# Kernel optimization log

Measured on AMD Instinct MI355X. Metric: run time of the kernel, lower is better.

## Reference

```python
import jax, jax.numpy as jnp
import numpy as np

N = 50000
E = 1600000
F_IN = 512
NHID = 32
LATENT = 16
NCLS = 16


def setup_inputs() -> dict:
    key = jax.random.key(0)
    ks = jax.random.split(key, 10)
    return {
        "features": jax.random.normal(ks[0], (N, F_IN), dtype=jnp.float32),
        "edge_src": jax.random.randint(ks[1], (E,), 0, N, dtype=jnp.int32),
        "edge_dst": jax.random.randint(ks[2], (E,), 0, N, dtype=jnp.int32),
        "edge_weight": jax.random.uniform(ks[3], (E,), dtype=jnp.float32),
        "W1": jax.random.normal(ks[4], (F_IN, NHID), dtype=jnp.float32) / np.sqrt(F_IN),
        "W2": jax.random.normal(ks[5], (NHID, LATENT), dtype=jnp.float32) / np.sqrt(NHID),
        "W3": jax.random.normal(ks[6], (LATENT, NCLS), dtype=jnp.float32) / np.sqrt(LATENT),
        "W4": jax.random.normal(ks[7], (NCLS, LATENT), dtype=jnp.float32) / np.sqrt(NCLS),
        "W5": jax.random.normal(ks[8], (LATENT, NHID), dtype=jnp.float32) / np.sqrt(LATENT),
        "W6": jax.random.normal(ks[9], (NHID, F_IN), dtype=jnp.float32) / np.sqrt(NHID),
    }


def gcn_conv(x, W, src, dst, w):
    # support = x @ W ; out = A_hat @ support (sparse aggregation over edges)
    support = x @ W                       # [N, out]
    msg = support[src] * w[:, None]       # [E, out]
    return jax.ops.segment_sum(msg, dst, num_segments=N)


def reference(features, edge_src, edge_dst, edge_weight, W1, W2, W3, W4, W5, W6):
    # dropout p=0.0 (eval semantics) -> identity
    x1 = jnp.tanh(gcn_conv(features, W1, edge_src, edge_dst, edge_weight))
    x2 = jnp.tanh(gcn_conv(x1, W2, edge_src, edge_dst, edge_weight))
    z = jnp.tanh(gcn_conv(x2, W3, edge_src, edge_dst, edge_weight))
    z2 = jnp.tanh(gcn_conv(z, W4, edge_src, edge_dst, edge_weight)) + x2
    z1 = jnp.tanh(gcn_conv(z2, W5, edge_src, edge_dst, edge_weight)) + x1
    feat_recon = jax.nn.sigmoid(gcn_conv(z1, W6, edge_src, edge_dst, edge_weight))
    pred = jax.nn.softmax(z, axis=1)
    return feat_recon, z, pred
```

## Files before the change

kernel.cpp:

```cpp
#include <hip/hip_runtime.h>
#include <hip/hip_bf16.h>
#include <math.h>

#define FIN 512
#define NHID 32
#define LAT 16
#define BCAP 16384

#define BR 128
#define KC 64
__global__ __launch_bounds__(256) void gemm_fin(const float* __restrict__ feat,
                                                const float* __restrict__ W,
                                                float* __restrict__ out0,
                                                float* __restrict__ out1,
                                                int n, int ntile) {
    __shared__ float xT[KC][BR];
    __shared__ float Wc[KC][NHID];
    const int tid = threadIdx.x;
    const int tile = blockIdx.x % ntile;
    const int khalf = blockIdx.x / ntile;
    const int r0 = tile * BR;
    const int k0 = khalf * 256;
    float* __restrict__ out = khalf ? out1 : out0;
    const int rt = tid >> 3;
    const int ct = tid & 7;
    const int srow = tid >> 4;
    const int sc4 = tid & 15;
    float acc[4][4] = {{0.f}};

    for (int kc = 0; kc < 256; kc += KC) {
        {
            const float4* wg = reinterpret_cast<const float4*>(W + (k0 + kc) * NHID);
            float4* wl = reinterpret_cast<float4*>(&Wc[0][0]);
            wl[tid] = wg[tid];
            wl[tid + 256] = wg[tid + 256];
        }
#pragma unroll
        for (int i = 0; i < 8; ++i) {
            int rr = srow + 16 * i;
            int r = r0 + rr;
            float4 v;
            if (r < n)
                v = *reinterpret_cast<const float4*>(feat + (size_t)r * FIN + k0 + kc + sc4 * 4);
            else
                v.x = v.y = v.z = v.w = 0.f;
            int gs = ((rr >> 2) ^ (sc4 & 7)) * 4 + (rr & 3);
            xT[sc4 * 4 + 0][gs] = v.x;
            xT[sc4 * 4 + 1][gs] = v.y;
            xT[sc4 * 4 + 2][gs] = v.z;
            xT[sc4 * 4 + 3][gs] = v.w;
        }
        __syncthreads();
#pragma unroll 4
        for (int k = 0; k < KC; ++k) {
            int sw = (rt ^ ((k >> 2) & 7)) * 4;
            float4 xv = *reinterpret_cast<const float4*>(&xT[k][sw]);
            float4 wv = *reinterpret_cast<const float4*>(&Wc[k][ct * 4]);
            acc[0][0] = fmaf(xv.x, wv.x, acc[0][0]);
            acc[0][1] = fmaf(xv.x, wv.y, acc[0][1]);
            acc[0][2] = fmaf(xv.x, wv.z, acc[0][2]);
            acc[0][3] = fmaf(xv.x, wv.w, acc[0][3]);
            acc[1][0] = fmaf(xv.y, wv.x, acc[1][0]);
            acc[1][1] = fmaf(xv.y, wv.y, acc[1][1]);
            acc[1][2] = fmaf(xv.y, wv.z, acc[1][2]);
            acc[1][3] = fmaf(xv.y, wv.w, acc[1][3]);
            acc[2][0] = fmaf(xv.z, wv.x, acc[2][0]);
            acc[2][1] = fmaf(xv.z, wv.y, acc[2][1]);
            acc[2][2] = fmaf(xv.z, wv.z, acc[2][2]);
            acc[2][3] = fmaf(xv.z, wv.w, acc[2][3]);
            acc[3][0] = fmaf(xv.w, wv.x, acc[3][0]);
            acc[3][1] = fmaf(xv.w, wv.y, acc[3][1]);
            acc[3][2] = fmaf(xv.w, wv.z, acc[3][2]);
            acc[3][3] = fmaf(xv.w, wv.w, acc[3][3]);
        }
        __syncthreads();
    }
#pragma unroll
    for (int i = 0; i < 4; ++i) {
        int r = r0 + rt * 4 + i;
        if (r < n) {
            float4 o;
            o.x = acc[i][0]; o.y = acc[i][1]; o.z = acc[i][2]; o.w = acc[i][3];
            *reinterpret_cast<float4*>(out + (size_t)r * NHID + ct * 4) = o;
        }
    }
}

__global__ __launch_bounds__(256) void add2(float* __restrict__ a,
                                            const float* __restrict__ b, int n4) {
    int i = blockIdx.x * 256 + threadIdx.x;
    if (i < n4) {
        float4 va = reinterpret_cast<float4*>(a)[i];
        float4 vb = reinterpret_cast<const float4*>(b)[i];
        va.x += vb.x; va.y += vb.y; va.z += vb.z; va.w += vb.w;
        reinterpret_cast<float4*>(a)[i] = va;
    }
}

__global__ __launch_bounds__(256) void binit(int* __restrict__ bcursor, int nb) {
    int t = threadIdx.x;
    if (t < nb) bcursor[t] = t * BCAP;
}

__global__ __launch_bounds__(256) void build_a(const int* __restrict__ src,
                                               const int* __restrict__ dst,
                                               const float* __restrict__ w,
                                               int* __restrict__ bcursor,
                                               unsigned long long* __restrict__ rec2,
                                               int e, int nb) {
    __shared__ int cnt[256];
    __shared__ int gb[256];
    const int tid = threadIdx.x;
    const int i0 = blockIdx.x * 4096;
    cnt[tid] = 0;
    __syncthreads();
    unsigned long long rc[16];
    int rkbk[16];
#pragma unroll
    for (int k = 0; k < 16; ++k) {
        int j = i0 + k * 256 + tid;
        rkbk[k] = -1;
        if (j < e) {
            int d = dst[j];
            int b = d >> 8;
            int rk = atomicAdd(&cnt[b], 1);
            rkbk[k] = (rk << 8) | b;
            rc[k] = ((unsigned long long)__float_as_uint(w[j]) << 32) |
                    ((unsigned)d << 16) | (unsigned)src[j];
        }
    }
    __syncthreads();
    if (tid < nb && cnt[tid] > 0) gb[tid] = atomicAdd(&bcursor[tid], cnt[tid]);
    __syncthreads();
#pragma unroll
    for (int k = 0; k < 16; ++k) {
        if (rkbk[k] >= 0) {
            int b = rkbk[k] & 255;
            int rk = rkbk[k] >> 8;
            rec2[gb[b] + rk] = rc[k];
        }
    }
}

__global__ __launch_bounds__(256) void build_b(const unsigned long long* __restrict__ rec2,
                                               const int* __restrict__ bcursor,
                                               int2* __restrict__ rp2,
                                               unsigned long long* __restrict__ rec,
                                               int n) {
    __shared__ int cnt[256];
    __shared__ int cur[256];
    const int t = threadIdx.x;
    const int b = blockIdx.x;
    const int lo = b * BCAP;
    const int hi = bcursor[b];
    cnt[t] = 0;
    __syncthreads();
    for (int i = lo + t; i < hi; i += 256)
        atomicAdd(&cnt[((unsigned)rec2[i] >> 16) & 255], 1);
    __syncthreads();
    int v = cnt[t];
    cur[t] = v;
    __syncthreads();
    for (int off = 1; off < 256; off <<= 1) {
        int x = (t >= off) ? cur[t - off] : 0;
        __syncthreads();
        cur[t] += x;
        __syncthreads();
    }
    int ex = cur[t] - v;
    int node = b * 256 + t;
    if (node < n) {
        int2 se; se.x = lo + ex; se.y = lo + ex + v;
        rp2[node] = se;
    }
    __syncthreads();
    cur[t] = ex;
    __syncthreads();
    for (int i = lo + t; i < hi; i += 256) {
        unsigned long long r = rec2[i];
        unsigned lo32 = (unsigned)r;
        int ln = (lo32 >> 16) & 255;
        int p = atomicAdd(&cur[ln], 1);
        rec[lo + p] = (r & 0xffffffff00000000ull) | (lo32 & 0xffffu);
    }
}

template <int NE, bool PRED, int D>
__device__ __forceinline__ void gath(const float* __restrict__ sq,
                                     const unsigned long long* __restrict__ rec,
                                     int e0, int end,
                                     float& ax, float& ay, float& az, float& aw) {
    unsigned long long r[NE];
#pragma unroll
    for (int j = 0; j < NE; ++j)
        r[j] = (!PRED || (e0 + 4 * j < end)) ? rec[e0 + 4 * j] : 0ull;
    float4 v[NE];
#pragma unroll
    for (int j = 0; j < NE; ++j)
        v[j] = *reinterpret_cast<const float4*>(sq + (size_t)(unsigned)(r[j] & 0xffffffffu) * D);
#pragma unroll
    for (int j = 0; j < NE; ++j) {
        float w = __uint_as_float((unsigned)(r[j] >> 32));
        ax = fmaf(v[j].x, w, ax); ay = fmaf(v[j].y, w, ay);
        az = fmaf(v[j].z, w, az); aw = fmaf(v[j].w, w, aw);
    }
}

template <int D, int C, int MODE, bool SMAX>
__global__ __launch_bounds__(256) void agg_fused(const float* __restrict__ s,
                                                 const unsigned long long* __restrict__ rec,
                                                 const int2* __restrict__ rp2,
                                                 const float* __restrict__ Wn,
                                                 const float* __restrict__ res,
                                                 float* __restrict__ out0,
                                                 float* __restrict__ out1,
                                                 float* __restrict__ pred, int n) {
    constexpr int CH = D / 4;
    __shared__ float wl[(MODE == 1 || MODE == 3) ? D * C : 1];
    if (MODE == 1 || MODE == 3) {
        for (int i = threadIdx.x; i < D * C; i += 256) wl[i] = Wn[i];
        __syncthreads();
    }
    constexpr int NPB = 256 / D;
    const int node = blockIdx.x * NPB + threadIdx.x / D;
    const int lane = threadIdx.x % D;
    const int q = lane & (CH - 1);
    const int st = lane / CH;
    float ax = 0.f, ay = 0.f, az = 0.f, aw = 0.f;
    if (node < n) {
        const float* sq = s + 4 * q;
        int2 se = rp2[node];
        int i = se.x;
        const int end = se.y;
        for (; i + 32 <= end; i += 32)
            gath<8, false, D>(sq, rec, i + st, end, ax, ay, az, aw);
        if (i + 16 <= end) {
            gath<4, false, D>(sq, rec, i + st, end, ax, ay, az, aw);
            i += 16;
        }
        if (i < end)
            gath<4, true, D>(sq, rec, i + st, end, ax, ay, az, aw);
    }
    ax += __shfl_xor(ax, CH, D);  ax += __shfl_xor(ax, 2 * CH, D);
    ay += __shfl_xor(ay, CH, D);  ay += __shfl_xor(ay, 2 * CH, D);
    az += __shfl_xor(az, CH, D);  az += __shfl_xor(az, 2 * CH, D);
    aw += __shfl_xor(aw, CH, D);  aw += __shfl_xor(aw, 2 * CH, D);

    if (MODE == 1) {
        float vx = tanhf(ax), vy = tanhf(ay), vz = tanhf(az), vw = tanhf(aw);
        if (node < n && st == 0) {
            float4 o; o.x = vx; o.y = vy; o.z = vz; o.w = vw;
            *reinterpret_cast<float4*>(out0 + (size_t)node * D + 4 * q) = o;
        }
        if (SMAX) {
            float m = fmaxf(fmaxf(vx, vy), fmaxf(vz, vw));
            m = fmaxf(m, __shfl_xor(m, 1, 16));
            m = fmaxf(m, __shfl_xor(m, 2, 16));
            float ex = expf(vx - m), ey = expf(vy - m), ez = expf(vz - m), ew = expf(vw - m);
            float sm = ex + ey + ez + ew;
            sm += __shfl_xor(sm, 1, 16);
            sm += __shfl_xor(sm, 2, 16);
            float inv = 1.f / sm;
            if (node < n && st == 0) {
                float4 o; o.x = ex * inv; o.y = ey * inv; o.z = ez * inv; o.w = ew * inv;
                *reinterpret_cast<float4*>(pred + (size_t)node * 16 + 4 * q) = o;
            }
        }
        const int cc = lane & (C - 1);
        float g = 0.f;
#pragma unroll
        for (int k = 0; k < D; ++k) {
            float comp = ((k & 3) == 0) ? vx : ((k & 3) == 1) ? vy : ((k & 3) == 2) ? vz : vw;
            float vk = __shfl(comp, k >> 2, D);
            g = fmaf(vk, wl[k * C + cc], g);
        }
        if (node < n && lane < C) out1[(size_t)node * C + cc] = g;
    } else if (MODE == 2) {
        if (node < n && st == 0) {
            float4 rv = *reinterpret_cast<const float4*>(res + (size_t)node * D + 4 * q);
            float4 o;
            o.x = tanhf(ax) + rv.x; o.y = tanhf(ay) + rv.y;
            o.z = tanhf(az) + rv.z; o.w = tanhf(aw) + rv.w;
            *reinterpret_cast<float4*>(out0 + (size_t)node * D + 4 * q) = o;
        }
    } else if (MODE == 3) {
        float g0 = 0.f, g1 = 0.f;
#pragma unroll
        for (int k = 0; k < 16; ++k) {
            float comp = ((k & 3) == 0) ? ax : ((k & 3) == 1) ? ay : ((k & 3) == 2) ? az : aw;
            float vk = __shfl(comp, k >> 2, 16);
            g0 = fmaf(vk, wl[k * 32 + lane], g0);
            g1 = fmaf(vk, wl[k * 32 + lane + 16], g1);
        }
        if (node < n) {
            out0[(size_t)node * 32 + lane] = tanhf(g0) + res[(size_t)node * 32 + lane];
            out0[(size_t)node * 32 + lane + 16] = tanhf(g1) + res[(size_t)node * 32 + lane + 16];
        }
    } else {
        if (node < n && st == 0) {
            float4 o; o.x = ax; o.y = ay; o.z = az; o.w = aw;
            *reinterpret_cast<float4*>(out0 + (size_t)node * D + 4 * q) = o;
        }
    }
}

#define FT_R 32
__global__ __launch_bounds__(256) void gemm_fout(const float* __restrict__ a,
                                                 const float* __restrict__ W,
                                                 float* __restrict__ out, int n,
                                                 int ntiles) {
    __shared__ float wl[NHID * 256];
    __shared__ float aT[NHID][FT_R + 1];
    const int part = blockIdx.x & 1;
    {
        const float4* w4 = reinterpret_cast<const float4*>(W);
        float4* wl4 = reinterpret_cast<float4*>(wl);
#pragma unroll
        for (int i = threadIdx.x; i < NHID * 64; i += 256) {
            int k = i >> 6;
            int j = i & 63;
            wl4[k * 64 + j] = w4[k * 128 + part * 64 + j];
        }
    }
    const int rt = threadIdx.x >> 5;
    const int ct = threadIdx.x & 31;
    const int srr = threadIdx.x >> 3;
    const int sk4 = threadIdx.x & 7;

    for (int tile = blockIdx.x >> 1; tile < ntiles; tile += gridDim.x >> 1) {
        const int r0 = tile * FT_R;
        __syncthreads();
        {
            int r = r0 + srr;
            float4 v;
            if (r < n)
                v = *reinterpret_cast<const float4*>(a + (size_t)r * NHID + sk4 * 4);
            else
                v.x = v.y = v.z = v.w = 0.f;
            aT[sk4 * 4 + 0][srr] = v.x;
            aT[sk4 * 4 + 1][srr] = v.y;
            aT[sk4 * 4 + 2][srr] = v.z;
            aT[sk4 * 4 + 3][srr] = v.w;
        }
        __syncthreads();
#pragma unroll
        for (int cc = 0; cc < 2; ++cc) {
            float acc[4][4] = {{0.f}};
#pragma unroll 8
            for (int k = 0; k < NHID; ++k) {
                float4 av = *reinterpret_cast<const float4*>(&aT[k][rt * 4]);
                float4 wv = *reinterpret_cast<const float4*>(&wl[k * 256 + cc * 128 + ct * 4]);
                acc[0][0] = fmaf(av.x, wv.x, acc[0][0]);
                acc[0][1] = fmaf(av.x, wv.y, acc[0][1]);
                acc[0][2] = fmaf(av.x, wv.z, acc[0][2]);
                acc[0][3] = fmaf(av.x, wv.w, acc[0][3]);
                acc[1][0] = fmaf(av.y, wv.x, acc[1][0]);
                acc[1][1] = fmaf(av.y, wv.y, acc[1][1]);
                acc[1][2] = fmaf(av.y, wv.z, acc[1][2]);
                acc[1][3] = fmaf(av.y, wv.w, acc[1][3]);
                acc[2][0] = fmaf(av.z, wv.x, acc[2][0]);
                acc[2][1] = fmaf(av.z, wv.y, acc[2][1]);
                acc[2][2] = fmaf(av.z, wv.z, acc[2][2]);
                acc[2][3] = fmaf(av.z, wv.w, acc[2][3]);
                acc[3][0] = fmaf(av.w, wv.x, acc[3][0]);
                acc[3][1] = fmaf(av.w, wv.y, acc[3][1]);
                acc[3][2] = fmaf(av.w, wv.z, acc[3][2]);
                acc[3][3] = fmaf(av.w, wv.w, acc[3][3]);
            }
#pragma unroll
            for (int i = 0; i < 4; ++i) {
                int r = r0 + rt * 4 + i;
                if (r < n) {
                    float4 o;
                    o.x = 1.f / (1.f + expf(-acc[i][0]));
                    o.y = 1.f / (1.f + expf(-acc[i][1]));
                    o.z = 1.f / (1.f + expf(-acc[i][2]));
                    o.w = 1.f / (1.f + expf(-acc[i][3]));
                    *reinterpret_cast<float4*>(out + (size_t)r * FIN + part * 256 + cc * 128 + ct * 4) = o;
                }
            }
        }
    }
}

extern "C" void kernel_launch(void* const* d_in, const int* in_sizes, int n_in,
                              void* d_out, int out_size, void* d_ws, size_t ws_size,
                              hipStream_t stream) {
    const float* feat = (const float*)d_in[0];
    const int* esrc = (const int*)d_in[1];
    const int* edst = (const int*)d_in[2];
    const float* ewt = (const float*)d_in[3];
    const float* W1 = (const float*)d_in[4];
    const float* W2 = (const float*)d_in[5];
    const float* W3 = (const float*)d_in[6];
    const float* W4 = (const float*)d_in[7];
    const float* W5 = (const float*)d_in[8];
    const float* W6 = (const float*)d_in[9];
    const int n = in_sizes[0] / FIN;
    const int e = in_sizes[1];
    const int nb = (n + 255) >> 8;

    float* out = (float*)d_out;
    float* recon = out;
    float* zout = out + (size_t)n * FIN;
    float* pred = zout + (size_t)n * 16;

    char* wsb = (char*)d_ws;
    const size_t captot = (size_t)nb * BCAP;
    unsigned long long* rec = (unsigned long long*)wsb;
    unsigned long long* rec2 = rec + captot;
    int2* rp2 = (int2*)(rec2 + captot);
    int* bcursor = (int*)(rp2 + n);
    size_t ioff = (size_t)((bcursor + nb) - (int*)wsb);
    ioff = (ioff + 3) & ~(size_t)3;
    float* S_a = (float*)wsb + ioff;
    float* S_b = S_a + (size_t)n * 32;
    float* X1 = S_b + (size_t)n * 32;
    float* X2 = X1 + (size_t)n * 32;
    float* G1 = X2 + (size_t)n * 16;

    const int geb = (e + 4095) / 4096;
    const int gn32 = (n + 7) / 8;
    const int gn16 = (n + 15) / 16;
    const int ntile1 = (n + BR - 1) / BR;
    const int ntiles6 = (n + FT_R - 1) / FT_R;

    binit<<<1, 256, 0, stream>>>(bcursor, nb);
    build_a<<<geb, 256, 0, stream>>>(esrc, edst, ewt, bcursor, rec2, e, nb);
    build_b<<<nb, 256, 0, stream>>>(rec2, bcursor, rp2, rec, n);

    gemm_fin<<<2 * ntile1, 256, 0, stream>>>(feat, W1, S_a, G1, n, ntile1);
    add2<<<(n * 32 / 4 + 255) / 256, 256, 0, stream>>>(S_a, G1, n * 32 / 4);
    agg_fused<32, 16, 1, false><<<gn32, 256, 0, stream>>>(S_a, rec, rp2, W2, nullptr, X1, S_b, nullptr, n);
    agg_fused<16, 16, 1, false><<<gn16, 256, 0, stream>>>(S_b, rec, rp2, W3, nullptr, X2, S_a, nullptr, n);
    agg_fused<16, 16, 1, true><<<gn16, 256, 0, stream>>>(S_a, rec, rp2, W4, nullptr, zout, S_b, pred, n);
    agg_fused<16, 16, 2, false><<<gn16, 256, 0, stream>>>(S_b, rec, rp2, nullptr, X2, S_a, nullptr, nullptr, n);
    agg_fused<16, 32, 3, false><<<gn16, 256, 0, stream>>>(S_a, rec, rp2, W5, X1, S_b, nullptr, nullptr, n);
    agg_fused<32, 32, 4, false><<<gn32, 256, 0, stream>>>(S_b, rec, rp2, nullptr, nullptr, S_a, nullptr, nullptr, n);
    gemm_fout<<<1024, 256, 0, stream>>>(S_a, W6, recon, n, ntiles6);
}
```

Measured before the change: 304.9 us.

## Split GEMMs into more K/column parts and stage bucket scatter in shared memory

The input GEMM now splits K into four parts instead of two, and a four-way add combines the partial sums, which raises block count for more parallelism. The output GEMM splits columns four ways with twice the grid, which shrinks per-block shared weight storage. build_a now does a prefix scan over bucket counts and stages records in shared memory grouped by bucket, so the global scatter writes are more contiguous. The trade-offs are extra partial-sum traffic for the K split and more shared memory plus barriers in build_a.

```diff
diff --git a/kernel.cpp b/kernel.cpp
--- a/kernel.cpp
+++ b/kernel.cpp
@@ -11,24 +11,26 @@
 #define KC 64
 __global__ __launch_bounds__(256) void gemm_fin(const float* __restrict__ feat,
                                                 const float* __restrict__ W,
-                                                float* __restrict__ out0,
-                                                float* __restrict__ out1,
+                                                float* __restrict__ o0,
+                                                float* __restrict__ o1,
+                                                float* __restrict__ o2,
+                                                float* __restrict__ o3,
                                                 int n, int ntile) {
     __shared__ float xT[KC][BR];
     __shared__ float Wc[KC][NHID];
     const int tid = threadIdx.x;
     const int tile = blockIdx.x % ntile;
-    const int khalf = blockIdx.x / ntile;
+    const int kq = blockIdx.x / ntile;
     const int r0 = tile * BR;
-    const int k0 = khalf * 256;
-    float* __restrict__ out = khalf ? out1 : out0;
+    const int k0 = kq * 128;
+    float* __restrict__ out = (kq == 0) ? o0 : (kq == 1) ? o1 : (kq == 2) ? o2 : o3;
     const int rt = tid >> 3;
     const int ct = tid & 7;
     const int srow = tid >> 4;
     const int sc4 = tid & 15;
     float acc[4][4] = {{0.f}};
 
-    for (int kc = 0; kc < 256; kc += KC) {
+    for (int kc = 0; kc < 128; kc += KC) {
         {
             const float4* wg = reinterpret_cast<const float4*>(W + (k0 + kc) * NHID);
             float4* wl = reinterpret_cast<float4*>(&Wc[0][0]);
@@ -86,13 +88,20 @@
     }
 }
 
-__global__ __launch_bounds__(256) void add2(float* __restrict__ a,
-                                            const float* __restrict__ b, int n4) {
+__global__ __launch_bounds__(256) void add4(float* __restrict__ a,
+                                            const float* __restrict__ b,
+                                            const float* __restrict__ c,
+                                            const float* __restrict__ d, int n4) {
     int i = blockIdx.x * 256 + threadIdx.x;
     if (i < n4) {
         float4 va = reinterpret_cast<float4*>(a)[i];
         float4 vb = reinterpret_cast<const float4*>(b)[i];
-        va.x += vb.x; va.y += vb.y; va.z += vb.z; va.w += vb.w;
+        float4 vc = reinterpret_cast<const float4*>(c)[i];
+        float4 vd = reinterpret_cast<const float4*>(d)[i];
+        va.x += vb.x + vc.x + vd.x;
+        va.y += vb.y + vc.y + vd.y;
+        va.z += vb.z + vc.z + vd.z;
+        va.w += vb.w + vc.w + vd.w;
         reinterpret_cast<float4*>(a)[i] = va;
     }
 }
@@ -109,7 +118,10 @@
                                                unsigned long long* __restrict__ rec2,
                                                int e, int nb) {
     __shared__ int cnt[256];
+    __shared__ int base[256];
     __shared__ int gb[256];
+    __shared__ unsigned long long lrec[4096];
+    __shared__ int gpos[4096];
     const int tid = threadIdx.x;
     const int i0 = blockIdx.x * 4096;
     cnt[tid] = 0;
@@ -130,16 +142,33 @@
         }
     }
     __syncthreads();
-    if (tid < nb && cnt[tid] > 0) gb[tid] = atomicAdd(&bcursor[tid], cnt[tid]);
+    const int v = cnt[tid];
+    base[tid] = v;
+    __syncthreads();
+    for (int off = 1; off < 256; off <<= 1) {
+        int x = (tid >= off) ? base[tid - off] : 0;
+        __syncthreads();
+        base[tid] += x;
+        __syncthreads();
+    }
+    const int ex = base[tid] - v;
+    __syncthreads();
+    base[tid] = ex;
+    if (tid < nb && v > 0) gb[tid] = atomicAdd(&bcursor[tid], v);
     __syncthreads();
 #pragma unroll
     for (int k = 0; k < 16; ++k) {
         if (rkbk[k] >= 0) {
             int b = rkbk[k] & 255;
             int rk = rkbk[k] >> 8;
-            rec2[gb[b] + rk] = rc[k];
-        }
-    }
+            int m = base[b] + rk;
+            lrec[m] = rc[k];
+            gpos[m] = gb[b] + rk;
+        }
+    }
+    __syncthreads();
+    const int total = (i0 + 4096 <= e) ? 4096 : (e - i0);
+    for (int m = tid; m < total; m += 256) rec2[gpos[m]] = lrec[m];
 }
 
 __global__ __launch_bounds__(256) void build_b(const unsigned long long* __restrict__ rec2,
@@ -309,17 +338,17 @@
                                                  const float* __restrict__ W,
                                                  float* __restrict__ out, int n,
                                                  int ntiles) {
-    __shared__ float wl[NHID * 256];
+    __shared__ float wl[NHID * 128];
     __shared__ float aT[NHID][FT_R + 1];
-    const int part = blockIdx.x & 1;
+    const int part = blockIdx.x & 3;
     {
         const float4* w4 = reinterpret_cast<const float4*>(W);
         float4* wl4 = reinterpret_cast<float4*>(wl);
 #pragma unroll
-        for (int i = threadIdx.x; i < NHID * 64; i += 256) {
-            int k = i >> 6;
-            int j = i & 63;
-            wl4[k * 64 + j] = w4[k * 128 + part * 64 + j];
+        for (int i = threadIdx.x; i < NHID * 32; i += 256) {
+            int k = i >> 5;
+            int j = i & 31;
+            wl4[k * 32 + j] = w4[k * 128 + part * 32 + j];
         }
     }
     const int rt = threadIdx.x >> 5;
@@ -327,7 +356,7 @@
     const int srr = threadIdx.x >> 3;
     const int sk4 = threadIdx.x & 7;
 
-    for (int tile = blockIdx.x >> 1; tile < ntiles; tile += gridDim.x >> 1) {
+    for (int tile = blockIdx.x >> 2; tile < ntiles; tile += gridDim.x >> 2) {
         const int r0 = tile * FT_R;
         __syncthreads();
         {
@@ -343,41 +372,38 @@
             aT[sk4 * 4 + 3][srr] = v.w;
         }
         __syncthreads();
-#pragma unroll
-        for (int cc = 0; cc < 2; ++cc) {
-            float acc[4][4] = {{0.f}};
+        float acc[4][4] = {{0.f}};
 #pragma unroll 8
-            for (int k = 0; k < NHID; ++k) {
-                float4 av = *reinterpret_cast<const float4*>(&aT[k][rt * 4]);
-                float4 wv = *reinterpret_cast<const float4*>(&wl[k * 256 + cc * 128 + ct * 4]);
-                acc[0][0] = fmaf(av.x, wv.x, acc[0][0]);
-                acc[0][1] = fmaf(av.x, wv.y, acc[0][1]);
-                acc[0][2] = fmaf(av.x, wv.z, acc[0][2]);
-                acc[0][3] = fmaf(av.x, wv.w, acc[0][3]);
-                acc[1][0] = fmaf(av.y, wv.x, acc[1][0]);
-                acc[1][1] = fmaf(av.y, wv.y, acc[1][1]);
-                acc[1][2] = fmaf(av.y, wv.z, acc[1][2]);
-                acc[1][3] = fmaf(av.y, wv.w, acc[1][3]);
-                acc[2][0] = fmaf(av.z, wv.x, acc[2][0]);
-                acc[2][1] = fmaf(av.z, wv.y, acc[2][1]);
-                acc[2][2] = fmaf(av.z, wv.z, acc[2][2]);
-                acc[2][3] = fmaf(av.z, wv.w, acc[2][3]);
-                acc[3][0] = fmaf(av.w, wv.x, acc[3][0]);
-                acc[3][1] = fmaf(av.w, wv.y, acc[3][1]);
-                acc[3][2] = fmaf(av.w, wv.z, acc[3][2]);
-                acc[3][3] = fmaf(av.w, wv.w, acc[3][3]);
-            }
-#pragma unroll
-            for (int i = 0; i < 4; ++i) {
-                int r = r0 + rt * 4 + i;
-                if (r < n) {
-                    float4 o;
-                    o.x = 1.f / (1.f + expf(-acc[i][0]));
-                    o.y = 1.f / (1.f + expf(-acc[i][1]));
-                    o.z = 1.f / (1.f + expf(-acc[i][2]));
-                    o.w = 1.f / (1.f + expf(-acc[i][3]));
-                    *reinterpret_cast<float4*>(out + (size_t)r * FIN + part * 256 + cc * 128 + ct * 4) = o;
-                }
+        for (int k = 0; k < NHID; ++k) {
+            float4 av = *reinterpret_cast<const float4*>(&aT[k][rt * 4]);
+            float4 wv = *reinterpret_cast<const float4*>(&wl[k * 128 + ct * 4]);
+            acc[0][0] = fmaf(av.x, wv.x, acc[0][0]);
+            acc[0][1] = fmaf(av.x, wv.y, acc[0][1]);
+            acc[0][2] = fmaf(av.x, wv.z, acc[0][2]);
+            acc[0][3] = fmaf(av.x, wv.w, acc[0][3]);
+            acc[1][0] = fmaf(av.y, wv.x, acc[1][0]);
+            acc[1][1] = fmaf(av.y, wv.y, acc[1][1]);
+            acc[1][2] = fmaf(av.y, wv.z, acc[1][2]);
+            acc[1][3] = fmaf(av.y, wv.w, acc[1][3]);
+            acc[2][0] = fmaf(av.z, wv.x, acc[2][0]);
+            acc[2][1] = fmaf(av.z, wv.y, acc[2][1]);
+            acc[2][2] = fmaf(av.z, wv.z, acc[2][2]);
+            acc[2][3] = fmaf(av.z, wv.w, acc[2][3]);
+            acc[3][0] = fmaf(av.w, wv.x, acc[3][0]);
+            acc[3][1] = fmaf(av.w, wv.y, acc[3][1]);
+            acc[3][2] = fmaf(av.w, wv.z, acc[3][2]);
+            acc[3][3] = fmaf(av.w, wv.w, acc[3][3]);
+        }
+#pragma unroll
+        for (int i = 0; i < 4; ++i) {
+            int r = r0 + rt * 4 + i;
+            if (r < n) {
+                float4 o;
+                o.x = 1.f / (1.f + expf(-acc[i][0]));
+                o.y = 1.f / (1.f + expf(-acc[i][1]));
+                o.z = 1.f / (1.f + expf(-acc[i][2]));
+                o.w = 1.f / (1.f + expf(-acc[i][3]));
+                *reinterpret_cast<float4*>(out + (size_t)r * FIN + part * 128 + ct * 4) = o;
             }
         }
     }
@@ -418,6 +444,8 @@
     float* X1 = S_b + (size_t)n * 32;
     float* X2 = X1 + (size_t)n * 32;
     float* G1 = X2 + (size_t)n * 16;
+    float* G2 = G1 + (size_t)n * 32;
+    float* G3 = G2 + (size_t)n * 32;
 
     const int geb = (e + 4095) / 4096;
     const int gn32 = (n + 7) / 8;
@@ -429,13 +457,13 @@
     build_a<<<geb, 256, 0, stream>>>(esrc, edst, ewt, bcursor, rec2, e, nb);
     build_b<<<nb, 256, 0, stream>>>(rec2, bcursor, rp2, rec, n);
 
-    gemm_fin<<<2 * ntile1, 256, 0, stream>>>(feat, W1, S_a, G1, n, ntile1);
-    add2<<<(n * 32 / 4 + 255) / 256, 256, 0, stream>>>(S_a, G1, n * 32 / 4);
+    gemm_fin<<<4 * ntile1, 256, 0, stream>>>(feat, W1, S_a, G1, G2, G3, n, ntile1);
+    add4<<<(n * 32 / 4 + 255) / 256, 256, 0, stream>>>(S_a, G1, G2, G3, n * 32 / 4);
     agg_fused<32, 16, 1, false><<<gn32, 256, 0, stream>>>(S_a, rec, rp2, W2, nullptr, X1, S_b, nullptr, n);
     agg_fused<16, 16, 1, false><<<gn16, 256, 0, stream>>>(S_b, rec, rp2, W3, nullptr, X2, S_a, nullptr, n);
     agg_fused<16, 16, 1, true><<<gn16, 256, 0, stream>>>(S_a, rec, rp2, W4, nullptr, zout, S_b, pred, n);
     agg_fused<16, 16, 2, false><<<gn16, 256, 0, stream>>>(S_b, rec, rp2, nullptr, X2, S_a, nullptr, nullptr, n);
     agg_fused<16, 32, 3, false><<<gn16, 256, 0, stream>>>(S_a, rec, rp2, W5, X1, S_b, nullptr, nullptr, n);
     agg_fused<32, 32, 4, false><<<gn32, 256, 0, stream>>>(S_b, rec, rp2, nullptr, nullptr, S_a, nullptr, nullptr, n);
-    gemm_fout<<<1024, 256, 0, stream>>>(S_a, W6, recon, n, ntiles6);
-}
+    gemm_fout<<<2048, 256, 0, stream>>>(S_a, W6, recon, n, ntiles6);
+}
```

After: 308.9 us. Within noise of the previous version (+1.3%).
